# Performance work log

Hardware: AMD Instinct MI355X
Metric: run time of the kernel (lower is better)

## Reference

```python
import jax, jax.numpy as jnp
import numpy as np

N_X, N_U, N_Y = 256, 32, 32
BATCH, T = 16, 8192
LAM_MIN, LAM_MAX = 0.9, 0.995
B_SCALE, D_SCALE = 0.25, 0.25


def setup_inputs() -> dict:
    key = jax.random.key(0)
    k = jax.random.split(key, 6)
    # Orthogonal Q via QR of a random Gaussian matrix (as in the torch module)
    M = jax.random.normal(k[0], (N_X, N_X), dtype=jnp.float32)
    Q, _ = jnp.linalg.qr(M)
    lam = LAM_MIN + (LAM_MAX - LAM_MIN) * jax.random.uniform(k[1], (N_X,), dtype=jnp.float32)
    Bmat = B_SCALE * jax.random.normal(k[2], (N_X, N_U), dtype=jnp.float32)
    # C picks out the first n_y coordinates (C[i, i] = 1)
    C = jnp.eye(N_Y, N_X, dtype=jnp.float32)
    D = D_SCALE * jax.random.normal(k[3], (N_Y, N_U), dtype=jnp.float32)
    x0 = jax.random.normal(k[4], (BATCH, N_X), dtype=jnp.float32)
    u = jax.random.normal(k[5], (BATCH, T, N_U), dtype=jnp.float32)
    return {"x0": x0, "u": u, "Q": Q, "lam": lam, "Bmat": Bmat, "C": C, "D": D}


def _diag_scan(lam, v):
    """Diagonal linear recurrence x_t = lam * x_{t-1} + v_t (x_0 folded into v[:, 0]).

    lam: (N,), v: (B, T, N) -> states x_1..x_T of shape (B, T, N).
    """
    a = jnp.broadcast_to(lam, v.shape)

    def op(l, r):
        a1, b1 = l
        a2, b2 = r
        return a1 * a2, a2 * b1 + b2

    return jax.lax.associative_scan(op, (a, v), axis=1)[1]


def reference(x0, u, Q, lam, Bmat, C, D):
    Bz = Q.T @ Bmat            # (n_x, n_u) modal input matrix
    Cz = C @ Q                 # (n_y, n_x) modal output matrix
    z0 = x0 @ Q                # (B, n_x)   modal initial state
    v = jnp.einsum('btu,nu->btn', u, Bz)   # (B, T, n_x)
    v = v.at[:, 0].add(lam * z0)            # fold lam * z0 into first step
    z_next = _diag_scan(lam, v)             # (B, T, n_x) = z_1..z_T
    # y_t uses z_t for t = 0..T-1 (states[:, :-1] in the original)
    z_prev = jnp.concatenate([z0[:, None, :], z_next[:, :-1]], axis=1)
    y = jnp.einsum('btn,yn->bty', z_prev, Cz) + jnp.einsum('btu,yu->bty', u, D)
    return y
```

## Files before the change

kernel.cpp:

```cpp
#include <hip/hip_runtime.h>

typedef _Float16 half4_t __attribute__((ext_vector_type(4)));
typedef _Float16 half8_t __attribute__((ext_vector_type(8)));
typedef float f32x4 __attribute__((ext_vector_type(4)));

constexpr int NX = 256, NU = 32, NY = 32, BATCH = 16, T = 8192;
constexpr int NC = 64, L = 128;
constexpr int SUBT = 32, NSUB = L / SUBT;
constexpr int ZP = 264;

__device__ __forceinline__ half8_t cvt8(float4 a, float4 b) {
    half8_t h;
    h[0] = (_Float16)a.x; h[1] = (_Float16)a.y; h[2] = (_Float16)a.z; h[3] = (_Float16)a.w;
    h[4] = (_Float16)b.x; h[5] = (_Float16)b.y; h[6] = (_Float16)b.z; h[7] = (_Float16)b.w;
    return h;
}

__global__ __launch_bounds__(256) void k_pre(
    const float* __restrict__ x0, const float* __restrict__ Q,
    const float* __restrict__ Bm,
    _Float16* __restrict__ Bzh, float* __restrict__ z0)
{
    int o = blockIdx.x * 64 + (threadIdx.x >> 2);
    int p = threadIdx.x & 3;
    if (o >= 12288) return;
    float s = 0.f;
    int k0 = p * 64;
    if (o < 8192) {
        int n = o >> 5, j = o & 31;
        for (int k = k0; k < k0 + 64; ++k) s = fmaf(Q[k * NX + n], Bm[k * NU + j], s);
    } else {
        int g = o - 8192; int b = g >> 8, nn = g & 255;
        for (int k = k0; k < k0 + 64; ++k) s = fmaf(x0[b * NX + k], Q[k * NX + nn], s);
    }
    s += __shfl_xor(s, 1);
    s += __shfl_xor(s, 2);
    if (p == 0) {
        if (o < 8192) Bzh[o] = (_Float16)s;
        else          z0[o - 8192] = s;
    }
}

__global__ __launch_bounds__(256) void k_phase1(
    const float* __restrict__ u, const float* __restrict__ lam,
    const _Float16* __restrict__ Bzh, float* __restrict__ S)
{
    __shared__ __align__(16) _Float16 ut[2][SUBT][32];

    const int b = blockIdx.x >> 6, c = blockIdx.x & 63, tid = threadIdx.x;
    const int w = tid >> 6, lane = tid & 63, m16 = lane & 15, quad = lane >> 4;

    half8_t bfrag[4];
    #pragma unroll
    for (int i = 0; i < 4; ++i)
        bfrag[i] = *(const half8_t*)&Bzh[((4 * w + i) * 16 + m16) * NU + quad * 8];

    float wr[4][4], wt16[4], l32[4], acc[4];
    #pragma unroll
    for (int i = 0; i < 4; ++i) {
        float la = lam[(4 * w + i) * 16 + m16];
        float p2 = la * la, p4 = p2 * p2, p8 = p4 * p4, p16 = p8 * p8;
        float inv1 = 1.0f / la;
        float inv4 = (inv1 * inv1) * (inv1 * inv1);
        float pq = 1.0f;
        if (quad & 1) pq *= inv4;
        if (quad & 2) pq *= inv4 * inv4;
        float w0 = (p16 * p8 * p4 * p2 * la) * pq;
        wr[i][0] = w0;
        wr[i][1] = w0 * inv1;
        wr[i][2] = wr[i][1] * inv1;
        wr[i][3] = wr[i][2] * inv1;
        wt16[i] = 1.0f / p16;
        l32[i] = p16 * p16;
        acc[i] = 0.f;
    }

    const float* ug = u + ((size_t)(b * T) + (size_t)c * L) * NU;

    for (int sub = 0; sub < NSUB; ++sub) {
        {
            float4 uu = *(const float4*)(ug + (size_t)sub * SUBT * NU + tid * 4);
            int tr = tid >> 3, cb = ((tid & 7) * 4 + (tr & 3) * 8) & 31;
            half4_t h; h.x = (_Float16)uu.x; h.y = (_Float16)uu.y;
            h.z = (_Float16)uu.z; h.w = (_Float16)uu.w;
            *(half4_t*)&ut[sub & 1][tr][cb] = h;
        }
        __syncthreads();
        int rot = (m16 & 3) * 8;
        half8_t af0 = *(const half8_t*)&ut[sub & 1][m16][(quad * 8 + rot) & 31];
        half8_t af1 = *(const half8_t*)&ut[sub & 1][16 + m16][(quad * 8 + rot) & 31];
        #pragma unroll
        for (int i = 0; i < 4; ++i) {
            f32x4 z4 = {0.f, 0.f, 0.f, 0.f};
            f32x4 v0 = __builtin_amdgcn_mfma_f32_16x16x32_f16(af0, bfrag[i], z4, 0, 0, 0);
            f32x4 v1 = __builtin_amdgcn_mfma_f32_16x16x32_f16(af1, bfrag[i], z4, 0, 0, 0);
            float s0 = wr[i][0] * v0[0] + wr[i][1] * v0[1] + wr[i][2] * v0[2] + wr[i][3] * v0[3];
            float s1 = wr[i][0] * v1[0] + wr[i][1] * v1[1] + wr[i][2] * v1[2] + wr[i][3] * v1[3];
            acc[i] = fmaf(l32[i], acc[i], fmaf(wt16[i], s1, s0));
        }
    }
    #pragma unroll
    for (int i = 0; i < 4; ++i) {
        acc[i] += __shfl_xor(acc[i], 16);
        acc[i] += __shfl_xor(acc[i], 32);
    }
    float out = quad == 0 ? acc[0] : quad == 1 ? acc[1] : quad == 2 ? acc[2] : acc[3];
    S[(size_t)blockIdx.x * NX + (4 * w + quad) * 16 + m16] = out;
}

__global__ __launch_bounds__(256) void k_phase3(
    const float* __restrict__ u, const float* __restrict__ lam,
    const _Float16* __restrict__ Bzh, const float* __restrict__ Q,
    const float* __restrict__ D, const float* __restrict__ S,
    const float* __restrict__ z0, float* __restrict__ y)
{
    __shared__ __align__(16) _Float16 ut[2][2][SUBT][32];
    __shared__ __align__(16) _Float16 zt[2][SUBT][ZP];
    __shared__ float pvec[2][NX];

    const int bx = blockIdx.x, b = bx >> 5, ci = bx & 31, tid = threadIdx.x;
    const int cA = 2 * ci, cB = 2 * ci + 1;
    const int w = tid >> 6, lane = tid & 63, m16 = lane & 15, quad = lane >> 4;
    const int tw = w & 1, yw = w >> 1;
    const int rot = (m16 & 3) * 8;
    const int tr = tid >> 3, cb = ((tid & 7) * 4 + (tr & 3) * 8) & 31;

    const float* ugA = u + ((size_t)(b * T) + (size_t)cA * L) * NU;
    const float* ugB = u + ((size_t)(b * T) + (size_t)cB * L) * NU;
    float4 ucA = *(const float4*)(ugA + tid * 4);
    float4 ucB = *(const float4*)(ugB + tid * 4);

    {
        float la = lam[tid];
        float l2L = 128.0f * __log2f(la);
        const float* Sb = S + (size_t)(b * NC) * NX + tid;
        float pv = 0.f;
        #pragma unroll 8
        for (int k = 0; k < cA; ++k) {
            float wgt = exp2f((float)k * l2L);
            pv = fmaf(wgt, Sb[(size_t)(cA - 1 - k) * NX], pv);
        }
        float pA = fmaf(exp2f((float)cA * l2L), z0[b * NX + tid], pv);
        pvec[0][tid] = pA;
        pvec[1][tid] = fmaf(exp2f(l2L), pA, Sb[(size_t)cA * NX]);
    }

    half8_t bfrag[4];
    #pragma unroll
    for (int i = 0; i < 4; ++i)
        bfrag[i] = *(const half8_t*)&Bzh[((4 * w + i) * 16 + m16) * NU + quad * 8];
    half8_t wfrag[9];
    #pragma unroll
    for (int kk = 0; kk < 8; ++kk) {
        float4 qa = *(const float4*)&Q[(size_t)(yw * 16 + m16) * NX + kk * 32 + quad * 8];
        float4 qb = *(const float4*)&Q[(size_t)(yw * 16 + m16) * NX + kk * 32 + quad * 8 + 4];
        wfrag[kk] = cvt8(qa, qb);
    }
    {
        float4 da = *(const float4*)&D[(size_t)(yw * 16 + m16) * NU + quad * 8];
        float4 db = *(const float4*)&D[(size_t)(yw * 16 + m16) * NU + quad * 8 + 4];
        wfrag[8] = cvt8(da, db);
    }

    float lamn[4], inv1[4], iq[4], i16p[4], fq[4], f16p[4], l32[4], pA[4], pB[4];
    #pragma unroll
    for (int i = 0; i < 4; ++i) {
        int ni = (4 * w + i) * 16 + m16;
        float la = lam[ni];
        lamn[i] = la;
        float p2 = la * la, p4 = p2 * p2, p8 = p4 * p4, p16 = p8 * p8;
        float iv = 1.0f / la;
        inv1[i] = iv;
        float iv4 = (iv * iv) * (iv * iv);
        float pqi = 1.0f, pqf = 1.0f;
        if (quad & 1) { pqi *= iv4; pqf *= p4; }
        if (quad & 2) { pqi *= iv4 * iv4; pqf *= p8; }
        iq[i] = iv * pqi;
        fq[i] = pqf;
        i16p[i] = 1.0f / p16;
        f16p[i] = p16;
        l32[i] = p16 * p16;
    }

    {
        half4_t hA; hA.x = (_Float16)ucA.x; hA.y = (_Float16)ucA.y;
        hA.z = (_Float16)ucA.z; hA.w = (_Float16)ucA.w;
        *(half4_t*)&ut[0][0][tr][cb] = hA;
        half4_t hB; hB.x = (_Float16)ucB.x; hB.y = (_Float16)ucB.y;
        hB.z = (_Float16)ucB.z; hB.w = (_Float16)ucB.w;
        *(half4_t*)&ut[1][0][tr][cb] = hB;
    }
    __syncthreads();
    #pragma unroll
    for (int i = 0; i < 4; ++i) {
        pA[i] = pvec[0][(4 * w + i) * 16 + m16];
        pB[i] = pvec[1][(4 * w + i) * 16 + m16];
    }
    float4 unA = *(const float4*)(ugA + (size_t)SUBT * NU + tid * 4);
    float4 unB = *(const float4*)(ugB + (size_t)SUBT * NU + tid * 4);

    float* ygA = y + ((size_t)(b * T) + (size_t)cA * L) * NY;
    float* ygB = y + ((size_t)(b * T) + (size_t)cB * L) * NY;

    half8_t afA0, afA1, afB0, afB1;

    for (int sub = 0; sub < NSUB; ++sub) {
        afA0 = *(const half8_t*)&ut[0][sub & 1][m16][(quad * 8 + rot) & 31];
        afA1 = *(const half8_t*)&ut[0][sub & 1][16 + m16][(quad * 8 + rot) & 31];
        afB0 = *(const half8_t*)&ut[1][sub & 1][m16][(quad * 8 + rot) & 31];
        afB1 = *(const half8_t*)&ut[1][sub & 1][16 + m16][(quad * 8 + rot) & 31];
        if (sub < NSUB - 2) {
            ucA = *(const float4*)(ugA + (size_t)(sub + 2) * SUBT * NU + tid * 4);
            ucB = *(const float4*)(ugB + (size_t)(sub + 2) * SUBT * NU + tid * 4);
        }
        #pragma unroll
        for (int st = 0; st < 2; ++st) {
            half8_t af0 = st ? afB0 : afA0;
            half8_t af1 = st ? afB1 : afA1;
            float*  pp  = st ? pB : pA;
            #pragma unroll
            for (int i = 0; i < 4; ++i) {
                int ni = (4 * w + i) * 16 + m16;
                f32x4 z4 = {0.f, 0.f, 0.f, 0.f};
                f32x4 v0 = __builtin_amdgcn_mfma_f32_16x16x32_f16(af0, bfrag[i], z4, 0, 0, 0);
                f32x4 v1 = __builtin_amdgcn_mfma_f32_16x16x32_f16(af1, bfrag[i], z4, 0, 0, 0);
                float a0[4], a1[4];
                float sc = iq[i];
                #pragma unroll
                for (int r = 0; r < 4; ++r) {
                    a0[r] = v0[r] * sc;
                    a1[r] = v1[r] * (sc * i16p[i]);
                    sc *= inv1[i];
                }
                float e0[4], e1[4];
                e0[0] = 0.f; e0[1] = a0[0]; e0[2] = e0[1] + a0[1]; e0[3] = e0[2] + a0[2];
                float S40 = e0[3] + a0[3];
                e1[0] = 0.f; e1[1] = a1[0]; e1[2] = e1[1] + a1[1]; e1[3] = e1[2] + a1[2];
                float S41 = e1[3] + a1[3];
                float incl0 = S40;
                float t0 = __shfl_up(incl0, 16); if (quad >= 1) incl0 += t0;
                t0 = __shfl_up(incl0, 32);       if (quad >= 2) incl0 += t0;
                float excl0 = incl0 - S40;
                float total0 = __shfl(incl0, 48 + m16);
                float incl1 = S41;
                float t1 = __shfl_up(incl1, 16); if (quad >= 1) incl1 += t1;
                t1 = __shfl_up(incl1, 32);       if (quad >= 2) incl1 += t1;
                float excl1 = incl1 - S41;
                float total1 = __shfl(incl1, 48 + m16);
                float f = fq[i];
                #pragma unroll
                for (int r = 0; r < 4; ++r) {
                    float zv0 = f * (pp[i] + (excl0 + e0[r]));
                    float zv1 = (f * f16p[i]) * (pp[i] + (total0 + excl1 + e1[r]));
                    zt[st][quad * 4 + r][ni] = (_Float16)zv0;
                    zt[st][16 + quad * 4 + r][ni] = (_Float16)zv1;
                    f *= lamn[i];
                }
                pp[i] = l32[i] * (pp[i] + (total0 + total1));
            }
        }
        if (sub < NSUB - 1) {
            half4_t hA; hA.x = (_Float16)unA.x; hA.y = (_Float16)unA.y;
            hA.z = (_Float16)unA.z; hA.w = (_Float16)unA.w;
            *(half4_t*)&ut[0][(sub + 1) & 1][tr][cb] = hA;
            half4_t hB; hB.x = (_Float16)unB.x; hB.y = (_Float16)unB.y;
            hB.z = (_Float16)unB.z; hB.w = (_Float16)unB.w;
            *(half4_t*)&ut[1][(sub + 1) & 1][tr][cb] = hB;
            unA = ucA; unB = ucB;
        }
        __syncthreads();

        #pragma unroll
        for (int st = 0; st < 2; ++st) {
            f32x4 acc = {0.f, 0.f, 0.f, 0.f};
            #pragma unroll
            for (int kk = 0; kk < 8; ++kk) {
                half8_t az = *(const half8_t*)&zt[st][tw * 16 + m16][kk * 32 + quad * 8];
                acc = __builtin_amdgcn_mfma_f32_16x16x32_f16(wfrag[kk], az, acc, 0, 0, 0);
            }
            {
                half8_t au = st ? (tw ? afB1 : afB0) : (tw ? afA1 : afA0);
                acc = __builtin_amdgcn_mfma_f32_16x16x32_f16(wfrag[8], au, acc, 0, 0, 0);
            }
            float* yg = st ? ygB : ygA;
            float4 v = make_float4(acc[0], acc[1], acc[2], acc[3]);
            *(float4*)&yg[(size_t)(sub * SUBT + tw * 16 + m16) * NY + yw * 16 + quad * 4] = v;
        }
        if (sub < NSUB - 1)
            __syncthreads();
    }
}

extern "C" void kernel_launch(void* const* d_in, const int* in_sizes, int n_in,
                              void* d_out, int out_size, void* d_ws, size_t ws_size,
                              hipStream_t stream) {
    (void)in_sizes; (void)n_in; (void)out_size; (void)ws_size;
    const float* x0  = (const float*)d_in[0];
    const float* u   = (const float*)d_in[1];
    const float* Q   = (const float*)d_in[2];
    const float* lam = (const float*)d_in[3];
    const float* Bm  = (const float*)d_in[4];
    const float* D   = (const float*)d_in[6];
    float* y = (float*)d_out;

    char* ws = (char*)d_ws;
    _Float16* Bzh = (_Float16*)(ws);
    float*    z0  = (float*)(ws + 16384);
    float*    S   = (float*)(ws + 32768);

    k_pre   <<<192, 256, 0, stream>>>(x0, Q, Bm, Bzh, z0);
    k_phase1<<<BATCH * NC, 256, 0, stream>>>(u, lam, Bzh, S);
    k_phase3<<<BATCH * NC / 2, 256, 0, stream>>>(u, lam, Bzh, Q, D, S, z0, y);
}
```

Baseline: 114.3 us.

## Process two chunks per block in phase1 with register-prefetched double buffering

New measurement: 114.9 us. No clear change (+0.6%).

```diff
diff --git a/kernel.cpp b/kernel.cpp
--- a/kernel.cpp
+++ b/kernel.cpp
@@ -45,17 +45,25 @@
     const float* __restrict__ u, const float* __restrict__ lam,
     const _Float16* __restrict__ Bzh, float* __restrict__ S)
 {
-    __shared__ __align__(16) _Float16 ut[2][SUBT][32];
-
-    const int b = blockIdx.x >> 6, c = blockIdx.x & 63, tid = threadIdx.x;
+    __shared__ __align__(16) _Float16 ut[2][2][SUBT][32];
+
+    const int bx = blockIdx.x, b = bx >> 5, ci = bx & 31, tid = threadIdx.x;
+    const int cA = 2 * ci, cB = 2 * ci + 1;
     const int w = tid >> 6, lane = tid & 63, m16 = lane & 15, quad = lane >> 4;
+    const int rot = (m16 & 3) * 8;
+    const int tr = tid >> 3, cb = ((tid & 7) * 4 + (tr & 3) * 8) & 31;
+
+    const float* ugA = u + ((size_t)(b * T) + (size_t)cA * L) * NU;
+    const float* ugB = u + ((size_t)(b * T) + (size_t)cB * L) * NU;
+    float4 ucA = *(const float4*)(ugA + tid * 4);
+    float4 ucB = *(const float4*)(ugB + tid * 4);
 
     half8_t bfrag[4];
     #pragma unroll
     for (int i = 0; i < 4; ++i)
         bfrag[i] = *(const half8_t*)&Bzh[((4 * w + i) * 16 + m16) * NU + quad * 8];
 
-    float wr[4][4], wt16[4], l32[4], acc[4];
+    float wr[4][4], wt16[4], l32[4], accA[4], accB[4];
     #pragma unroll
     for (int i = 0; i < 4; ++i) {
         float la = lam[(4 * w + i) * 16 + m16];
@@ -72,40 +80,67 @@
         wr[i][3] = wr[i][2] * inv1;
         wt16[i] = 1.0f / p16;
         l32[i] = p16 * p16;
-        acc[i] = 0.f;
-    }
-
-    const float* ug = u + ((size_t)(b * T) + (size_t)c * L) * NU;
+        accA[i] = 0.f; accB[i] = 0.f;
+    }
+
+    {
+        half4_t hA; hA.x = (_Float16)ucA.x; hA.y = (_Float16)ucA.y;
+        hA.z = (_Float16)ucA.z; hA.w = (_Float16)ucA.w;
+        *(half4_t*)&ut[0][0][tr][cb] = hA;
+        half4_t hB; hB.x = (_Float16)ucB.x; hB.y = (_Float16)ucB.y;
+        hB.z = (_Float16)ucB.z; hB.w = (_Float16)ucB.w;
+        *(half4_t*)&ut[1][0][tr][cb] = hB;
+    }
+    __syncthreads();
+    float4 unA = *(const float4*)(ugA + (size_t)SUBT * NU + tid * 4);
+    float4 unB = *(const float4*)(ugB + (size_t)SUBT * NU + tid * 4);
 
     for (int sub = 0; sub < NSUB; ++sub) {
-        {
-            float4 uu = *(const float4*)(ug + (size_t)sub * SUBT * NU + tid * 4);
-            int tr = tid >> 3, cb = ((tid & 7) * 4 + (tr & 3) * 8) & 31;
-            half4_t h; h.x = (_Float16)uu.x; h.y = (_Float16)uu.y;
-            h.z = (_Float16)uu.z; h.w = (_Float16)uu.w;
-            *(half4_t*)&ut[sub & 1][tr][cb] = h;
-        }
-        __syncthreads();
-        int rot = (m16 & 3) * 8;
-        half8_t af0 = *(const half8_t*)&ut[sub & 1][m16][(quad * 8 + rot) & 31];
-        half8_t af1 = *(const half8_t*)&ut[sub & 1][16 + m16][(quad * 8 + rot) & 31];
+        half8_t afA0 = *(const half8_t*)&ut[0][sub & 1][m16][(quad * 8 + rot) & 31];
+        half8_t afA1 = *(const half8_t*)&ut[0][sub & 1][16 + m16][(quad * 8 + rot) & 31];
+        half8_t afB0 = *(const half8_t*)&ut[1][sub & 1][m16][(quad * 8 + rot) & 31];
+        half8_t afB1 = *(const half8_t*)&ut[1][sub & 1][16 + m16][(quad * 8 + rot) & 31];
+        if (sub < NSUB - 2) {
+            ucA = *(const float4*)(ugA + (size_t)(sub + 2) * SUBT * NU + tid * 4);
+            ucB = *(const float4*)(ugB + (size_t)(sub + 2) * SUBT * NU + tid * 4);
+        }
         #pragma unroll
         for (int i = 0; i < 4; ++i) {
             f32x4 z4 = {0.f, 0.f, 0.f, 0.f};
-            f32x4 v0 = __builtin_amdgcn_mfma_f32_16x16x32_f16(af0, bfrag[i], z4, 0, 0, 0);
-            f32x4 v1 = __builtin_amdgcn_mfma_f32_16x16x32_f16(af1, bfrag[i], z4, 0, 0, 0);
-            float s0 = wr[i][0] * v0[0] + wr[i][1] * v0[1] + wr[i][2] * v0[2] + wr[i][3] * v0[3];
-            float s1 = wr[i][0] * v1[0] + wr[i][1] * v1[1] + wr[i][2] * v1[2] + wr[i][3] * v1[3];
-            acc[i] = fmaf(l32[i], acc[i], fmaf(wt16[i], s1, s0));
+            f32x4 vA0 = __builtin_amdgcn_mfma_f32_16x16x32_f16(afA0, bfrag[i], z4, 0, 0, 0);
+            f32x4 vA1 = __builtin_amdgcn_mfma_f32_16x16x32_f16(afA1, bfrag[i], z4, 0, 0, 0);
+            f32x4 vB0 = __builtin_amdgcn_mfma_f32_16x16x32_f16(afB0, bfrag[i], z4, 0, 0, 0);
+            f32x4 vB1 = __builtin_amdgcn_mfma_f32_16x16x32_f16(afB1, bfrag[i], z4, 0, 0, 0);
+            float sA0 = wr[i][0] * vA0[0] + wr[i][1] * vA0[1] + wr[i][2] * vA0[2] + wr[i][3] * vA0[3];
+            float sA1 = wr[i][0] * vA1[0] + wr[i][1] * vA1[1] + wr[i][2] * vA1[2] + wr[i][3] * vA1[3];
+            float sB0 = wr[i][0] * vB0[0] + wr[i][1] * vB0[1] + wr[i][2] * vB0[2] + wr[i][3] * vB0[3];
+            float sB1 = wr[i][0] * vB1[0] + wr[i][1] * vB1[1] + wr[i][2] * vB1[2] + wr[i][3] * vB1[3];
+            accA[i] = fmaf(l32[i], accA[i], fmaf(wt16[i], sA1, sA0));
+            accB[i] = fmaf(l32[i], accB[i], fmaf(wt16[i], sB1, sB0));
+        }
+        if (sub < NSUB - 1) {
+            half4_t hA; hA.x = (_Float16)unA.x; hA.y = (_Float16)unA.y;
+            hA.z = (_Float16)unA.z; hA.w = (_Float16)unA.w;
+            *(half4_t*)&ut[0][(sub + 1) & 1][tr][cb] = hA;
+            half4_t hB; hB.x = (_Float16)unB.x; hB.y = (_Float16)unB.y;
+            hB.z = (_Float16)unB.z; hB.w = (_Float16)unB.w;
+            *(half4_t*)&ut[1][(sub + 1) & 1][tr][cb] = hB;
+            unA = ucA; unB = ucB;
+            __syncthreads();
         }
     }
     #pragma unroll
     for (int i = 0; i < 4; ++i) {
-        acc[i] += __shfl_xor(acc[i], 16);
-        acc[i] += __shfl_xor(acc[i], 32);
-    }
-    float out = quad == 0 ? acc[0] : quad == 1 ? acc[1] : quad == 2 ? acc[2] : acc[3];
-    S[(size_t)blockIdx.x * NX + (4 * w + quad) * 16 + m16] = out;
+        accA[i] += __shfl_xor(accA[i], 16);
+        accA[i] += __shfl_xor(accA[i], 32);
+        accB[i] += __shfl_xor(accB[i], 16);
+        accB[i] += __shfl_xor(accB[i], 32);
+    }
+    float outA = quad == 0 ? accA[0] : quad == 1 ? accA[1] : quad == 2 ? accA[2] : accA[3];
+    float outB = quad == 0 ? accB[0] : quad == 1 ? accB[1] : quad == 2 ? accB[2] : accB[3];
+    int nout = (4 * w + quad) * 16 + m16;
+    S[(size_t)(b * NC + cA) * NX + nout] = outA;
+    S[(size_t)(b * NC + cB) * NX + nout] = outB;
 }
 
 __global__ __launch_bounds__(256) void k_phase3(
@@ -309,6 +344,6 @@
     float*    S   = (float*)(ws + 32768);
 
     k_pre   <<<192, 256, 0, stream>>>(x0, Q, Bm, Bzh, z0);
-    k_phase1<<<BATCH * NC, 256, 0, stream>>>(u, lam, Bzh, S);
+    k_phase1<<<BATCH * NC / 2, 256, 0, stream>>>(u, lam, Bzh, S);
     k_phase3<<<BATCH * NC / 2, 256, 0, stream>>>(u, lam, Bzh, Q, D, S, z0, y);
 }
```
